# Optimization experiments

Measured on AMD Instinct MI355X. Metric: run time of the kernel, lower is better.

The kernel has to match this reference:

```python
import jax, jax.numpy as jnp
import numpy as np

B, S, E, H, L, F, V = 8, 1024, 768, 12, 6, 3072, 32000
HD = E // H  # head_dim = 64
EPS = 1e-5


def _pos_encoding(max_len, dim):
    pos = np.arange(max_len, dtype=np.float32)[:, None]
    div = np.exp(np.arange(0, dim, 2, dtype=np.float32) * (-np.log(10000.0) / dim))
    pe = np.zeros((max_len, dim), dtype=np.float32)
    pe[:, 0::2] = np.sin(pos * div)
    pe[:, 1::2] = np.cos(pos * div)
    return jnp.asarray(pe)


def setup_inputs() -> dict:
    key = jax.random.key(0)
    ks = jax.random.split(key, 16)
    sd = 0.02
    inp = {}
    inp['input_ids'] = jax.random.randint(ks[0], (B, S), 0, V)
    inp['attention_mask'] = jnp.ones((B, S), dtype=jnp.int32)
    inp['emb'] = jax.random.normal(ks[1], (V, E), jnp.float32) * sd
    inp['pe'] = _pos_encoding(S, E)
    inp['Wq'] = jax.random.normal(ks[2], (L, E, E), jnp.float32) * sd
    inp['bq'] = jnp.zeros((L, E), jnp.float32)
    inp['Wk'] = jax.random.normal(ks[3], (L, E, E), jnp.float32) * sd
    inp['bk'] = jnp.zeros((L, E), jnp.float32)
    inp['Wv'] = jax.random.normal(ks[4], (L, E, E), jnp.float32) * sd
    inp['bv'] = jnp.zeros((L, E), jnp.float32)
    inp['Wo'] = jax.random.normal(ks[5], (L, E, E), jnp.float32) * sd
    inp['bo'] = jnp.zeros((L, E), jnp.float32)
    inp['ln1_g'] = jnp.ones((L, E), jnp.float32)
    inp['ln1_b'] = jnp.zeros((L, E), jnp.float32)
    inp['W1'] = jax.random.normal(ks[6], (L, E, F), jnp.float32) * sd
    inp['b1'] = jnp.zeros((L, F), jnp.float32)
    inp['W2'] = jax.random.normal(ks[7], (L, F, E), jnp.float32) * sd
    inp['b2'] = jnp.zeros((L, E), jnp.float32)
    inp['ln2_g'] = jnp.ones((L, E), jnp.float32)
    inp['ln2_b'] = jnp.zeros((L, E), jnp.float32)
    inp['Wc'] = jax.random.normal(ks[8], (E, 2), jnp.float32) * sd
    inp['bc'] = jnp.zeros((2,), jnp.float32)
    return inp


def _layernorm(x, g, b):
    mu = jnp.mean(x, axis=-1, keepdims=True)
    var = jnp.mean(jnp.square(x - mu), axis=-1, keepdims=True)
    return (x - mu) * jax.lax.rsqrt(var + EPS) * g + b


def reference(input_ids, attention_mask, emb, pe, Wq, bq, Wk, bk, Wv, bv, Wo, bo,
              ln1_g, ln1_b, W1, b1, W2, b2, ln2_g, ln2_b, Wc, bc):
    x = emb[input_ids] + pe[None, :S, :]           # [B,S,E] (dropout = eval identity)
    mask = attention_mask[:, None, None, :]        # [B,1,1,S]
    scale = jnp.sqrt(jnp.float32(HD))

    def block(x, p):
        wq, bq_, wk, bk_, wv, bv_, wo, bo_, g1, be1, w1, b1_, w2, b2_, g2, be2 = p
        q = (x @ wq + bq_).reshape(B, S, H, HD).transpose(0, 2, 1, 3)  # [B,H,S,D]
        k = (x @ wk + bk_).reshape(B, S, H, HD).transpose(0, 2, 1, 3)
        v = (x @ wv + bv_).reshape(B, S, H, HD).transpose(0, 2, 1, 3)
        scores = jnp.einsum('bhsd,bhtd->bhst', q, k) / scale          # [B,H,S,S]
        scores = jnp.where(mask == 0, -jnp.inf, scores)
        attn = jax.nn.softmax(scores, axis=-1)
        o = jnp.einsum('bhst,bhtd->bhsd', attn, v)
        o = o.transpose(0, 2, 1, 3).reshape(B, S, E) @ wo + bo_
        x = _layernorm(x + o, g1, be1)
        ffn = jax.nn.relu(x @ w1 + b1_) @ w2 + b2_
        x = _layernorm(x + ffn, g2, be2)
        return x, None

    params = (Wq, bq, Wk, bk, Wv, bv, Wo, bo, ln1_g, ln1_b, W1, b1, W2, b2, ln2_g, ln2_b)
    x, _ = jax.lax.scan(block, x, params)
    pooled = jnp.mean(x, axis=1)                   # [B,E]
    return pooled @ Wc + bc                        # [B,2]
```

## Files before the change

### kernel.cpp

```cpp
#include <hip/hip_runtime.h>

typedef __bf16 bf16x8 __attribute__((ext_vector_type(8)));
typedef float  f32x4  __attribute__((ext_vector_type(4)));

constexpr int Bb = 8, Ss = 1024, Ee = 768, Hh = 12, Ll = 6, Ff = 3072;
constexpr int TOK  = Bb * Ss;
constexpr int NQKV = 3 * Ee;

static __device__ __forceinline__ f32x4 mfma16(bf16x8 a, bf16x8 b, f32x4 c) {
  return __builtin_amdgcn_mfma_f32_16x16x32_bf16(a, b, c, 0, 0, 0);
}

static __device__ __forceinline__ void async16(const void* g, void* l) {
  __builtin_amdgcn_global_load_lds(
      (const __attribute__((address_space(1))) unsigned int*)g,
      (__attribute__((address_space(3))) unsigned int*)l, 16, 0, 0);
}

static __device__ __forceinline__ bf16x8 ds_read128(const __bf16* p) {
  bf16x8 r;
  unsigned a = (unsigned)(size_t)p;
  asm volatile("ds_read_b128 %0, %1" : "=v"(r) : "v"(a));
  return r;
}

static __device__ __forceinline__ float fexp2(float x) {
  float r; asm("v_exp_f32 %0, %1" : "=v"(r) : "v"(x)); return r;
}

__global__ __launch_bounds__(256) void embed_kernel(
    const int* __restrict__ ids, const float* __restrict__ emb,
    const float* __restrict__ pe, float* __restrict__ x, __bf16* __restrict__ xb)
{
  int tok = blockIdx.x;
  int s   = tok & (Ss - 1);
  int id  = ids[tok];
  const float* er = emb + (size_t)id * Ee;
  const float* pr = pe  + (size_t)s  * Ee;
  size_t base = (size_t)tok * Ee;
#pragma unroll
  for (int i = 0; i < 3; i++) {
    int e = threadIdx.x + i * 256;
    float v = er[e] + pr[e];
    x[base + e]  = v;
    xb[base + e] = (__bf16)v;
  }
}

__global__ __launch_bounds__(256) void transpose_w_kernel(
    const float* __restrict__ src, __bf16* __restrict__ dst,
    int K, int N, size_t sls, size_t dls)
{
  __shared__ float t[32][33];
  src += (size_t)blockIdx.z * sls;
  dst += (size_t)blockIdx.z * dls;
  int n0 = blockIdx.x * 32, k0 = blockIdx.y * 32;
  int c = threadIdx.x & 31, r0 = threadIdx.x >> 5;
#pragma unroll
  for (int rr = 0; rr < 32; rr += 8)
    t[r0 + rr][c] = src[(size_t)(k0 + r0 + rr) * N + n0 + c];
  __syncthreads();
#pragma unroll
  for (int rr = 0; rr < 32; rr += 8)
    dst[(size_t)(n0 + r0 + rr) * K + k0 + c] = (__bf16)t[c][r0 + rr];
}

template<bool OUT_BF16, bool RELU>
__global__ __launch_bounds__(256, 3) void gemm_kernel(
    const __bf16* __restrict__ A, const __bf16* __restrict__ Bt,
    const float* __restrict__ bias0, const float* __restrict__ bias1,
    const float* __restrict__ bias2, int bseg,
    float* __restrict__ Cf, __bf16* __restrict__ Cb, int M, int N, int K)
{
  __shared__ __align__(16) __bf16 lA[3][64 * 64];
  __shared__ __align__(16) __bf16 lB[3][64 * 64];
  const int tid  = threadIdx.x;
  const int wave = tid >> 6, lane = tid & 63;
  const int quad = lane >> 4, c16 = lane & 15;
  const int wm = wave >> 1, wn = wave & 1;

  const int bid = blockIdx.x;
  const int xcd = bid & 7;
  const int lb  = bid >> 3;
  const int mb  = xcd * 8 + (lb & 7);
  const int nb  = lb >> 3;
  const size_t m0 = (size_t)mb * 128, n0 = (size_t)nb * 128;

  f32x4 acc[4][4] = {};

  const int s0l = tid >> 3;
  const int s0c = tid & 7;
  const int l0  = s0c ^ (s0l & 7);
  const int tr0 = (s0l << 1) | (l0 >> 2);
  const int gc0 = (l0 & 3) * 8;
  const int s1l = (tid + 256) >> 3;
  const int l1  = s0c ^ (s1l & 7);
  const int tr1 = (s1l << 1) | (l1 >> 2);
  const int gc1 = (l1 & 3) * 8;

  const __bf16* Ag0 = A  + (m0 + tr0) * K + gc0;
  const __bf16* Ag1 = A  + (m0 + tr1) * K + gc1;
  const __bf16* Bg0 = Bt + (n0 + tr0) * K + gc0;
  const __bf16* Bg1 = Bt + (n0 + tr1) * K + gc1;
  const int d0 = tid * 8;

  const int nk = K >> 5;

  auto stage = [&](int t, int slot) {
    const int kof = t << 5;
    async16(Ag0 + kof, &lA[slot][d0]);
    async16(Ag1 + kof, &lA[slot][d0 + 2048]);
    async16(Bg0 + kof, &lB[slot][d0]);
    async16(Bg1 + kof, &lB[slot][d0 + 2048]);
  };

  int aoff[4], boff[4];
#pragma unroll
  for (int f = 0; f < 4; f++) {
    int ra = wm * 64 + f * 16 + c16;
    int ja = ra >> 1;
    aoff[f] = ja * 64 + (((((ra & 1) << 2) | quad)) ^ (ja & 7)) * 8;
    int rb = wn * 64 + f * 16 + c16;
    int jb = rb >> 1;
    boff[f] = jb * 64 + (((((rb & 1) << 2) | quad)) ^ (jb & 7)) * 8;
  }

  stage(0, 0);
  stage(1, 1);
  asm volatile("s_waitcnt vmcnt(4)" ::: "memory");
  __builtin_amdgcn_s_barrier();
  __builtin_amdgcn_sched_barrier(0);

  int slot = 0;
  for (int t = 0; t < nk; ++t) {
    if (t + 2 < nk) {
      int ns = slot + 2; if (ns >= 3) ns -= 3;
      stage(t + 2, ns);
    }
    const __bf16* la = &lA[slot][0];
    const __bf16* lb = &lB[slot][0];
    bf16x8 af[4], bfr[4];
#pragma unroll
    for (int f = 0; f < 4; f++) af[f]  = ds_read128(la + aoff[f]);
#pragma unroll
    for (int f = 0; f < 4; f++) bfr[f] = ds_read128(lb + boff[f]);
    asm volatile("s_waitcnt lgkmcnt(0)" ::: "memory");
    __builtin_amdgcn_sched_barrier(0);
    __builtin_amdgcn_s_setprio(1);
#pragma unroll
    for (int mi = 0; mi < 4; mi++)
#pragma unroll
      for (int ni = 0; ni < 4; ni++)
        acc[mi][ni] = mfma16(af[mi], bfr[ni], acc[mi][ni]);
    __builtin_amdgcn_s_setprio(0);
    __builtin_amdgcn_sched_barrier(0);
    if (t + 2 < nk) asm volatile("s_waitcnt vmcnt(4)" ::: "memory");
    else            asm volatile("s_waitcnt vmcnt(0)" ::: "memory");
    __builtin_amdgcn_s_barrier();
    __builtin_amdgcn_sched_barrier(0);
    slot = (slot + 1 == 3) ? 0 : slot + 1;
  }

#pragma unroll
  for (int ni = 0; ni < 4; ni++) {
    int col = (int)n0 + wn * 64 + ni * 16 + c16;
    const float* bp = bias0;
    int cc = col;
    if (cc >= bseg) { bp = bias1; cc -= bseg; }
    if (cc >= bseg) { bp = bias2; cc -= bseg; }
    float bv = bp[cc];
#pragma unroll
    for (int mi = 0; mi < 4; mi++) {
#pragma unroll
      for (int rr = 0; rr < 4; rr++) {
        size_t row = m0 + wm * 64 + mi * 16 + quad * 4 + rr;
        float v = acc[mi][ni][rr] + bv;
        if (RELU) v = fmaxf(v, 0.f);
        if (OUT_BF16) Cb[row * N + col] = (__bf16)v;
        else          Cf[row * N + col] = v;
      }
    }
  }
}

__global__ __launch_bounds__(256, 4) void gemm64_kernel(
    const __bf16* __restrict__ A, const __bf16* __restrict__ Bt,
    const float* __restrict__ bias0,
    float* __restrict__ Cf, int N, int K)
{
  __shared__ __align__(16) __bf16 lA[3][32 * 64];
  __shared__ __align__(16) __bf16 lB[3][64 * 64];
  const int tid  = threadIdx.x;
  const int lane = tid & 63, wn = tid >> 6;
  const int quad = lane >> 4, c16 = lane & 15;

  const int bid = blockIdx.x;
  const int xcd = bid & 7;
  const int lb  = bid >> 3;
  const int mb  = xcd * 16 + (lb & 15);
  const int nb  = lb >> 4;
  const size_t m0 = (size_t)mb * 64, n0 = (size_t)nb * 128;

  f32x4 acc[4][2] = {};

  const int alr = tid >> 3, asc = tid & 7;
  const int al  = asc ^ (alr & 7);
  const int atr = (alr << 1) | (al >> 2);
  const int agc = (al & 3) * 8;
  const __bf16* Ag = A + (m0 + atr) * (size_t)K + agc;
  const int s0l = tid >> 3;
  const int s0c = tid & 7;
  const int l0  = s0c ^ (s0l & 7);
  const int tr0 = (s0l << 1) | (l0 >> 2);
  const int gc0 = (l0 & 3) * 8;
  const int s1l = (tid + 256) >> 3;
  const int l1  = s0c ^ (s1l & 7);
  const int tr1 = (s1l << 1) | (l1 >> 2);
  const int gc1 = (l1 & 3) * 8;
  const __bf16* Bg0 = Bt + (n0 + tr0) * (size_t)K + gc0;
  const __bf16* Bg1 = Bt + (n0 + tr1) * (size_t)K + gc1;
  const int d0 = tid * 8;

  const int nk = K >> 5;

  auto stage = [&](int t, int slot) {
    const int kof = t << 5;
    async16(Ag  + kof, &lA[slot][d0]);
    async16(Bg0 + kof, &lB[slot][d0]);
    async16(Bg1 + kof, &lB[slot][d0 + 2048]);
  };

  int aoff[4], boff[2];
#pragma unroll
  for (int f = 0; f < 4; f++) {
    int ra = f * 16 + c16;
    int ja = ra >> 1;
    aoff[f] = ja * 64 + ((((ra & 1) << 2) | quad) ^ (ja & 7)) * 8;
  }
#pragma unroll
  for (int f = 0; f < 2; f++) {
    int rb = wn * 32 + f * 16 + c16;
    int jb = rb >> 1;
    boff[f] = jb * 64 + ((((rb & 1) << 2) | quad) ^ (jb & 7)) * 8;
  }

  stage(0, 0);
  stage(1, 1);
  asm volatile("s_waitcnt vmcnt(3)" ::: "memory");
  __builtin_amdgcn_s_barrier();
  __builtin_amdgcn_sched_barrier(0);

  int slot = 0;
  for (int t = 0; t < nk; ++t) {
    if (t + 2 < nk) {
      int ns = slot + 2; if (ns >= 3) ns -= 3;
      stage(t + 2, ns);
    }
    const __bf16* la = &lA[slot][0];
    const __bf16* lb = &lB[slot][0];
    bf16x8 af[4], bfr[2];
#pragma unroll
    for (int f = 0; f < 4; f++) af[f]  = ds_read128(la + aoff[f]);
#pragma unroll
    for (int f = 0; f < 2; f++) bfr[f] = ds_read128(lb + boff[f]);
    asm volatile("s_waitcnt lgkmcnt(0)" ::: "memory");
    __builtin_amdgcn_sched_barrier(0);
    __builtin_amdgcn_s_setprio(1);
#pragma unroll
    for (int mi = 0; mi < 4; mi++)
#pragma unroll
      for (int ni = 0; ni < 2; ni++)
        acc[mi][ni] = mfma16(af[mi], bfr[ni], acc[mi][ni]);
    __builtin_amdgcn_s_setprio(0);
    __builtin_amdgcn_sched_barrier(0);
    if (t + 2 < nk) asm volatile("s_waitcnt vmcnt(3)" ::: "memory");
    else            asm volatile("s_waitcnt vmcnt(0)" ::: "memory");
    __builtin_amdgcn_s_barrier();
    __builtin_amdgcn_sched_barrier(0);
    slot = (slot + 1 == 3) ? 0 : slot + 1;
  }

#pragma unroll
  for (int ni = 0; ni < 2; ni++) {
    int col = (int)n0 + wn * 32 + ni * 16 + c16;
    float bv = bias0[col];
#pragma unroll
    for (int mi = 0; mi < 4; mi++) {
#pragma unroll
      for (int rr = 0; rr < 4; rr++) {
        size_t row = m0 + mi * 16 + quad * 4 + rr;
        Cf[row * N + col] = acc[mi][ni][rr] + bv;
      }
    }
  }
}

__global__ __launch_bounds__(256) void vtrans_kernel(
    const __bf16* __restrict__ qkv, __bf16* __restrict__ vt)
{
  int tid  = blockIdx.x * 256 + threadIdx.x;
  int d    = tid & 63;
  int rest = tid >> 6;
  int sc   = rest & 127;
  int bh   = rest >> 7;
  int b = bh / Hh, h = bh % Hh;
  const __bf16* src = qkv + (size_t)(b * Ss + sc * 8) * NQKV + 2 * Ee + h * 64 + d;
  bf16x8 v;
#pragma unroll
  for (int i = 0; i < 8; i++) v[i] = src[(size_t)i * NQKV];
  *(bf16x8*)(vt + ((size_t)bh * 64 + d) * Ss + sc * 8) = v;
}

__global__ __launch_bounds__(512, 6) void attn_kernel(
    const __bf16* __restrict__ qkv, const __bf16* __restrict__ vt,
    const int* __restrict__ amask, __bf16* __restrict__ out)
{
  __shared__ __align__(16) __bf16 kbuf[2][64 * 64];
  __shared__ __align__(16) __bf16 vbuf[2][64 * 64];
  __shared__ __align__(16) __bf16 plds[8][16 * 68];
  const int idx = blockIdx.x;
  const int bh = idx % 96, qi = idx / 96;
  const int b = bh / Hh, h = bh % Hh;
  const int lane = threadIdx.x & 63, wave = threadIdx.x >> 6;
  const int quad = lane >> 4, c16 = lane & 15;
  const int q0 = qi * 128 + wave * 16;

  const __bf16* qbase = qkv + (size_t)(b * Ss + q0 + c16) * NQKV + h * 64 + quad * 8;
  bf16x8 qf0 = *(const bf16x8*)(qbase);
  bf16x8 qf1 = *(const bf16x8*)(qbase + 32);

  const int srow = threadIdx.x >> 3;
  const int scol = ((threadIdx.x & 7) ^ (srow & 7)) * 8;
  const __bf16* kg = qkv + (size_t)(b * Ss + srow) * NQKV + Ee + h * 64 + scol;
  const __bf16* vg = vt + ((size_t)bh * 64 + srow) * Ss + scol;

  const int sa8 = c16 & 7;
  const int rc0 = (quad ^ sa8) * 8;
  const int rc1 = ((quad + 4) ^ sa8) * 8;

  f32x4 o[4] = {};
  float lrow[4] = {0.f, 0.f, 0.f, 0.f};
  const int* mp = amask + b * Ss;
  __bf16* pw = &plds[wave][0];
  const float CE = 0.18033688f;

  async16(kg, &kbuf[0][(size_t)threadIdx.x * 8]);
  async16(vg, &vbuf[0][(size_t)threadIdx.x * 8]);

  for (int t = 0; t < 16; t++) {
    const int tb = t * 64;
    __syncthreads();
    if (t < 15) {
      const int nb = (t + 1) & 1, ntb = tb + 64;
      async16(kg + (size_t)ntb * NQKV, &kbuf[nb][(size_t)threadIdx.x * 8]);
      async16(vg + ntb,                &vbuf[nb][(size_t)threadIdx.x * 8]);
    }
    const __bf16* kb = &kbuf[t & 1][0];
    const __bf16* vb = &vbuf[t & 1][0];

    float mk2[4];
#pragma unroll
    for (int n = 0; n < 4; n++) mk2[n] = mp[tb + n * 16 + c16] ? 0.f : -1e30f;
    bf16x8 kf[8], vf[8];
#pragma unroll
    for (int n = 0; n < 4; n++) {
      kf[2*n]   = *(const bf16x8*)(kb + (n * 16 + c16) * 64 + rc0);
      kf[2*n+1] = *(const bf16x8*)(kb + (n * 16 + c16) * 64 + rc1);
    }
#pragma unroll
    for (int n = 0; n < 4; n++) {
      vf[2*n]   = *(const bf16x8*)(vb + (n * 16 + c16) * 64 + rc0);
      vf[2*n+1] = *(const bf16x8*)(vb + (n * 16 + c16) * 64 + rc1);
    }

    f32x4 s[4];
#pragma unroll
    for (int n = 0; n < 4; n++) {
      f32x4 z = {};
      z = mfma16(qf0, kf[2*n], z);
      s[n] = mfma16(qf1, kf[2*n+1], z);
    }

#pragma unroll
    for (int rr = 0; rr < 4; rr++) {
      float p0 = fexp2(fmaf(s[0][rr], CE, mk2[0]));
      float p1 = fexp2(fmaf(s[1][rr], CE, mk2[1]));
      float p2 = fexp2(fmaf(s[2][rr], CE, mk2[2]));
      float p3 = fexp2(fmaf(s[3][rr], CE, mk2[3]));
      lrow[rr] += (p0 + p1) + (p2 + p3);
      int prow = (quad * 4 + rr) * 68;
      pw[prow + 0  + c16] = (__bf16)p0;
      pw[prow + 16 + c16] = (__bf16)p1;
      pw[prow + 32 + c16] = (__bf16)p2;
      pw[prow + 48 + c16] = (__bf16)p3;
    }

    bf16x8 pf0 = *(const bf16x8*)(pw + c16 * 68 + quad * 8);
    bf16x8 pf1 = *(const bf16x8*)(pw + c16 * 68 + 32 + quad * 8);
#pragma unroll
    for (int ni = 0; ni < 4; ni++) {
      o[ni] = mfma16(pf0, vf[2*ni],   o[ni]);
      o[ni] = mfma16(pf1, vf[2*ni+1], o[ni]);
    }
  }

#pragma unroll
  for (int rr = 0; rr < 4; rr++) {
    float sr = lrow[rr];
    sr += __shfl_xor(sr, 1);
    sr += __shfl_xor(sr, 2);
    sr += __shfl_xor(sr, 4);
    sr += __shfl_xor(sr, 8);
    float inv = 1.f / sr;
    size_t row = (size_t)(b * Ss + q0 + quad * 4 + rr) * Ee + h * 64;
    out[row + 0  + c16] = (__bf16)(o[0][rr] * inv);
    out[row + 16 + c16] = (__bf16)(o[1][rr] * inv);
    out[row + 32 + c16] = (__bf16)(o[2][rr] * inv);
    out[row + 48 + c16] = (__bf16)(o[3][rr] * inv);
  }
}

__global__ __launch_bounds__(256) void add_ln_kernel(
    const float* __restrict__ xin, const float* __restrict__ tmp,
    const float* __restrict__ g, const float* __restrict__ beta,
    float* __restrict__ xout, __bf16* __restrict__ xbout)
{
  __shared__ float red[8];
  size_t base = (size_t)blockIdx.x * Ee;
  float hv[3], s = 0.f, sq = 0.f;
#pragma unroll
  for (int i = 0; i < 3; i++) {
    int e = threadIdx.x + i * 256;
    hv[i] = xin[base + e] + tmp[base + e];
    s += hv[i]; sq += hv[i] * hv[i];
  }
#pragma unroll
  for (int m = 1; m < 64; m <<= 1) { s += __shfl_xor(s, m); sq += __shfl_xor(sq, m); }
  int wave = threadIdx.x >> 6;
  if ((threadIdx.x & 63) == 0) { red[wave] = s; red[4 + wave] = sq; }
  __syncthreads();
  s  = red[0] + red[1] + red[2] + red[3];
  sq = red[4] + red[5] + red[6] + red[7];
  float mean = s * (1.f / Ee);
  float var  = sq * (1.f / Ee) - mean * mean;
  float rstd = rsqrtf(var + 1e-5f);
#pragma unroll
  for (int i = 0; i < 3; i++) {
    int e = threadIdx.x + i * 256;
    float v = (hv[i] - mean) * rstd * g[e] + beta[e];
    xout[base + e]  = v;
    xbout[base + e] = (__bf16)v;
  }
}

__global__ __launch_bounds__(256) void pool1_kernel(
    const float* __restrict__ x, float* __restrict__ partial)
{
  int b = blockIdx.x, chunk = blockIdx.y;
  float acc[3] = {0.f, 0.f, 0.f};
  for (int s = chunk * 64; s < chunk * 64 + 64; s++) {
#pragma unroll
    for (int i = 0; i < 3; i++) {
      int e = threadIdx.x + i * 256;
      acc[i] += x[((size_t)b * Ss + s) * Ee + e];
    }
  }
#pragma unroll
  for (int i = 0; i < 3; i++) {
    int e = threadIdx.x + i * 256;
    partial[((size_t)b * 16 + chunk) * Ee + e] = acc[i];
  }
}

__global__ __launch_bounds__(256) void pool2_kernel(
    const float* __restrict__ partial, const float* __restrict__ Wc,
    const float* __restrict__ bc, float* __restrict__ out)
{
  __shared__ float red[8];
  int b = blockIdx.x;
  float p0 = 0.f, p1 = 0.f;
#pragma unroll
  for (int i = 0; i < 3; i++) {
    int e = threadIdx.x + i * 256;
    float pe_ = 0.f;
#pragma unroll
    for (int c = 0; c < 16; c++) pe_ += partial[((size_t)b * 16 + c) * Ee + e];
    pe_ *= (1.f / Ss);
    p0 += pe_ * Wc[e * 2 + 0];
    p1 += pe_ * Wc[e * 2 + 1];
  }
#pragma unroll
  for (int m = 1; m < 64; m <<= 1) { p0 += __shfl_xor(p0, m); p1 += __shfl_xor(p1, m); }
  int wave = threadIdx.x >> 6;
  if ((threadIdx.x & 63) == 0) { red[wave] = p0; red[4 + wave] = p1; }
  __syncthreads();
  if (threadIdx.x == 0) {
    out[b * 2 + 0] = red[0] + red[1] + red[2] + red[3] + bc[0];
    out[b * 2 + 1] = red[4] + red[5] + red[6] + red[7] + bc[1];
  }
}

extern "C" void kernel_launch(void* const* d_in, const int* in_sizes, int n_in,
                              void* d_out, int out_size, void* d_ws, size_t ws_size,
                              hipStream_t stream) {
  const int*   ids   = (const int*)  d_in[0];
  const int*   amask = (const int*)  d_in[1];
  const float* emb   = (const float*)d_in[2];
  const float* pe    = (const float*)d_in[3];
  const float* Wq    = (const float*)d_in[4];
  const float* bq    = (const float*)d_in[5];
  const float* Wk    = (const float*)d_in[6];
  const float* bk    = (const float*)d_in[7];
  const float* Wv    = (const float*)d_in[8];
  const float* bv    = (const float*)d_in[9];
  const float* Wo    = (const float*)d_in[10];
  const float* bo    = (const float*)d_in[11];
  const float* ln1g  = (const float*)d_in[12];
  const float* ln1b  = (const float*)d_in[13];
  const float* W1    = (const float*)d_in[14];
  const float* b1    = (const float*)d_in[15];
  const float* W2    = (const float*)d_in[16];
  const float* b2    = (const float*)d_in[17];
  const float* ln2g  = (const float*)d_in[18];
  const float* ln2b  = (const float*)d_in[19];
  const float* Wc    = (const float*)d_in[20];
  const float* bc    = (const float*)d_in[21];
  float* outp = (float*)d_out;

  char* p = (char*)d_ws;
  auto alloc = [&](size_t bytes) { char* r = p; p += (bytes + 255) & ~(size_t)255; return r; };
  float*  x     = (float*) alloc((size_t)TOK * Ee * 4);
  __bf16* xb    = (__bf16*)alloc((size_t)TOK * Ee * 2);
  float*  tmp   = (float*) alloc((size_t)TOK * Ee * 4);
  __bf16* attn  = (__bf16*)alloc((size_t)TOK * Ee * 2);
  char*   r1    = alloc((size_t)TOK * Ff * 2);
  __bf16* qkv   = (__bf16*)r1;
  __bf16* vt    = (__bf16*)(r1 + (size_t)TOK * NQKV * 2);
  __bf16* h1    = (__bf16*)r1;
  __bf16* wqkvt = (__bf16*)alloc((size_t)Ll * NQKV * Ee * 2);
  __bf16* wot   = (__bf16*)alloc((size_t)Ll * Ee * Ee * 2);
  __bf16* w1t   = (__bf16*)alloc((size_t)Ll * Ff * Ee * 2);
  __bf16* w2t   = (__bf16*)alloc((size_t)Ll * Ee * Ff * 2);
  float*  part  = (float*) alloc((size_t)Bb * 16 * Ee * 4);

  embed_kernel<<<TOK, 256, 0, stream>>>(ids, emb, pe, x, xb);

  transpose_w_kernel<<<dim3(Ee/32, Ee/32, Ll), 256, 0, stream>>>(
      Wq, wqkvt,                         Ee, Ee, (size_t)Ee*Ee, (size_t)NQKV*Ee);
  transpose_w_kernel<<<dim3(Ee/32, Ee/32, Ll), 256, 0, stream>>>(
      Wk, wqkvt + (size_t)Ee*Ee,         Ee, Ee, (size_t)Ee*Ee, (size_t)NQKV*Ee);
  transpose_w_kernel<<<dim3(Ee/32, Ee/32, Ll), 256, 0, stream>>>(
      Wv, wqkvt + (size_t)2*Ee*Ee,       Ee, Ee, (size_t)Ee*Ee, (size_t)NQKV*Ee);
  transpose_w_kernel<<<dim3(Ee/32, Ee/32, Ll), 256, 0, stream>>>(
      Wo, wot,                           Ee, Ee, (size_t)Ee*Ee, (size_t)Ee*Ee);
  transpose_w_kernel<<<dim3(Ff/32, Ee/32, Ll), 256, 0, stream>>>(
      W1, w1t,                           Ee, Ff, (size_t)Ee*Ff, (size_t)Ff*Ee);
  transpose_w_kernel<<<dim3(Ee/32, Ff/32, Ll), 256, 0, stream>>>(
      W2, w2t,                           Ff, Ee, (size_t)Ff*Ee, (size_t)Ee*Ff);

  for (int l = 0; l < Ll; l++) {
    gemm_kernel<true, false><<<64 * (NQKV/128), 256, 0, stream>>>(
        xb, wqkvt + (size_t)l*NQKV*Ee,
        bq + l*Ee, bk + l*Ee, bv + l*Ee, Ee,
        nullptr, qkv, TOK, NQKV, Ee);
    vtrans_kernel<<<3072, 256, 0, stream>>>(qkv, vt);
    attn_kernel<<<768, 512, 0, stream>>>(qkv, vt, amask, attn);
    gemm64_kernel<<<768, 256, 0, stream>>>(
        attn, wot + (size_t)l*Ee*Ee, bo + l*Ee, tmp, Ee, Ee);
    add_ln_kernel<<<TOK, 256, 0, stream>>>(x, tmp, ln1g + l*Ee, ln1b + l*Ee, x, xb);
    gemm_kernel<true, true><<<64 * (Ff/128), 256, 0, stream>>>(
        xb, w1t + (size_t)l*Ff*Ee,
        b1 + l*Ff, b1 + l*Ff, b1 + l*Ff, Ff,
        nullptr, h1, TOK, Ff, Ee);
    gemm64_kernel<<<768, 256, 0, stream>>>(
        h1, w2t + (size_t)l*Ee*Ff, b2 + l*Ee, tmp, Ee, Ff);
    add_ln_kernel<<<TOK, 256, 0, stream>>>(x, tmp, ln2g + l*Ee, ln2b + l*Ee, x, xb);
  }

  pool1_kernel<<<dim3(Bb, 16), 256, 0, stream>>>(x, part);
  pool2_kernel<<<Bb, 256, 0, stream>>>(part, Wc, bc, outp);
}
```

Before: 1.989 ms.

## Replace 64x128 4-wave N=768 GEMM with 128x128 8-wave tile kernel

```diff
diff --git a/kernel.cpp b/kernel.cpp
--- a/kernel.cpp
+++ b/kernel.cpp
@@ -183,70 +183,60 @@
   }
 }
 
-__global__ __launch_bounds__(256, 4) void gemm64_kernel(
+__global__ __launch_bounds__(512, 6) void gemm8w_kernel(
     const __bf16* __restrict__ A, const __bf16* __restrict__ Bt,
     const float* __restrict__ bias0,
     float* __restrict__ Cf, int N, int K)
 {
-  __shared__ __align__(16) __bf16 lA[3][32 * 64];
+  __shared__ __align__(16) __bf16 lA[3][64 * 64];
   __shared__ __align__(16) __bf16 lB[3][64 * 64];
   const int tid  = threadIdx.x;
-  const int lane = tid & 63, wn = tid >> 6;
+  const int wave = tid >> 6, lane = tid & 63;
   const int quad = lane >> 4, c16 = lane & 15;
+  const int wm = wave >> 1, wn = wave & 1;
 
   const int bid = blockIdx.x;
   const int xcd = bid & 7;
   const int lb  = bid >> 3;
-  const int mb  = xcd * 16 + (lb & 15);
-  const int nb  = lb >> 4;
-  const size_t m0 = (size_t)mb * 64, n0 = (size_t)nb * 128;
-
-  f32x4 acc[4][2] = {};
-
-  const int alr = tid >> 3, asc = tid & 7;
-  const int al  = asc ^ (alr & 7);
-  const int atr = (alr << 1) | (al >> 2);
-  const int agc = (al & 3) * 8;
-  const __bf16* Ag = A + (m0 + atr) * (size_t)K + agc;
-  const int s0l = tid >> 3;
-  const int s0c = tid & 7;
-  const int l0  = s0c ^ (s0l & 7);
-  const int tr0 = (s0l << 1) | (l0 >> 2);
-  const int gc0 = (l0 & 3) * 8;
-  const int s1l = (tid + 256) >> 3;
-  const int l1  = s0c ^ (s1l & 7);
-  const int tr1 = (s1l << 1) | (l1 >> 2);
-  const int gc1 = (l1 & 3) * 8;
-  const __bf16* Bg0 = Bt + (n0 + tr0) * (size_t)K + gc0;
-  const __bf16* Bg1 = Bt + (n0 + tr1) * (size_t)K + gc1;
+  const int mb  = xcd * 8 + (lb & 7);
+  const int nb  = lb >> 3;
+  const size_t m0 = (size_t)mb * 128, n0 = (size_t)nb * 128;
+
+  f32x4 acc[2][4] = {};
+
+  const int slr = tid >> 3, ssc = tid & 7;
+  const int sl  = ssc ^ (slr & 7);
+  const int str = (slr << 1) | (sl >> 2);
+  const int sgc = (sl & 3) * 8;
+  const __bf16* Ag = A  + (m0 + str) * (size_t)K + sgc;
+  const __bf16* Bg = Bt + (n0 + str) * (size_t)K + sgc;
   const int d0 = tid * 8;
 
   const int nk = K >> 5;
 
   auto stage = [&](int t, int slot) {
     const int kof = t << 5;
-    async16(Ag  + kof, &lA[slot][d0]);
-    async16(Bg0 + kof, &lB[slot][d0]);
-    async16(Bg1 + kof, &lB[slot][d0 + 2048]);
+    async16(Ag + kof, &lA[slot][d0]);
+    async16(Bg + kof, &lB[slot][d0]);
   };
 
-  int aoff[4], boff[2];
-#pragma unroll
-  for (int f = 0; f < 4; f++) {
-    int ra = f * 16 + c16;
+  int aoff[2], boff[4];
+#pragma unroll
+  for (int f = 0; f < 2; f++) {
+    int ra = wm * 32 + f * 16 + c16;
     int ja = ra >> 1;
     aoff[f] = ja * 64 + ((((ra & 1) << 2) | quad) ^ (ja & 7)) * 8;
   }
 #pragma unroll
-  for (int f = 0; f < 2; f++) {
-    int rb = wn * 32 + f * 16 + c16;
+  for (int f = 0; f < 4; f++) {
+    int rb = wn * 64 + f * 16 + c16;
     int jb = rb >> 1;
     boff[f] = jb * 64 + ((((rb & 1) << 2) | quad) ^ (jb & 7)) * 8;
   }
 
   stage(0, 0);
   stage(1, 1);
-  asm volatile("s_waitcnt vmcnt(3)" ::: "memory");
+  asm volatile("s_waitcnt vmcnt(2)" ::: "memory");
   __builtin_amdgcn_s_barrier();
   __builtin_amdgcn_sched_barrier(0);
 
@@ -258,22 +248,22 @@
     }
     const __bf16* la = &lA[slot][0];
     const __bf16* lb = &lB[slot][0];
-    bf16x8 af[4], bfr[2];
-#pragma unroll
-    for (int f = 0; f < 4; f++) af[f]  = ds_read128(la + aoff[f]);
-#pragma unroll
-    for (int f = 0; f < 2; f++) bfr[f] = ds_read128(lb + boff[f]);
+    bf16x8 af[2], bfr[4];
+#pragma unroll
+    for (int f = 0; f < 2; f++) af[f]  = ds_read128(la + aoff[f]);
+#pragma unroll
+    for (int f = 0; f < 4; f++) bfr[f] = ds_read128(lb + boff[f]);
     asm volatile("s_waitcnt lgkmcnt(0)" ::: "memory");
     __builtin_amdgcn_sched_barrier(0);
     __builtin_amdgcn_s_setprio(1);
 #pragma unroll
-    for (int mi = 0; mi < 4; mi++)
-#pragma unroll
-      for (int ni = 0; ni < 2; ni++)
+    for (int mi = 0; mi < 2; mi++)
+#pragma unroll
+      for (int ni = 0; ni < 4; ni++)
         acc[mi][ni] = mfma16(af[mi], bfr[ni], acc[mi][ni]);
     __builtin_amdgcn_s_setprio(0);
     __builtin_amdgcn_sched_barrier(0);
-    if (t + 2 < nk) asm volatile("s_waitcnt vmcnt(3)" ::: "memory");
+    if (t + 2 < nk) asm volatile("s_waitcnt vmcnt(2)" ::: "memory");
     else            asm volatile("s_waitcnt vmcnt(0)" ::: "memory");
     __builtin_amdgcn_s_barrier();
     __builtin_amdgcn_sched_barrier(0);
@@ -281,14 +271,14 @@
   }
 
 #pragma unroll
-  for (int ni = 0; ni < 2; ni++) {
-    int col = (int)n0 + wn * 32 + ni * 16 + c16;
+  for (int ni = 0; ni < 4; ni++) {
+    int col = (int)n0 + wn * 64 + ni * 16 + c16;
     float bv = bias0[col];
 #pragma unroll
-    for (int mi = 0; mi < 4; mi++) {
+    for (int mi = 0; mi < 2; mi++) {
 #pragma unroll
       for (int rr = 0; rr < 4; rr++) {
-        size_t row = m0 + mi * 16 + quad * 4 + rr;
+        size_t row = m0 + wm * 32 + mi * 16 + quad * 4 + rr;
         Cf[row * N + col] = acc[mi][ni][rr] + bv;
       }
     }
@@ -565,14 +555,14 @@
         nullptr, qkv, TOK, NQKV, Ee);
     vtrans_kernel<<<3072, 256, 0, stream>>>(qkv, vt);
     attn_kernel<<<768, 512, 0, stream>>>(qkv, vt, amask, attn);
-    gemm64_kernel<<<768, 256, 0, stream>>>(
+    gemm8w_kernel<<<64 * (Ee/128), 512, 0, stream>>>(
         attn, wot + (size_t)l*Ee*Ee, bo + l*Ee, tmp, Ee, Ee);
     add_ln_kernel<<<TOK, 256, 0, stream>>>(x, tmp, ln1g + l*Ee, ln1b + l*Ee, x, xb);
     gemm_kernel<true, true><<<64 * (Ff/128), 256, 0, stream>>>(
         xb, w1t + (size_t)l*Ff*Ee,
         b1 + l*Ff, b1 + l*Ff, b1 + l*Ff, Ff,
         nullptr, h1, TOK, Ff, Ee);
-    gemm64_kernel<<<768, 256, 0, stream>>>(
+    gemm8w_kernel<<<64 * (Ee/128), 512, 0, stream>>>(
         h1, w2t + (size_t)l*Ee*Ff, b2 + l*Ee, tmp, Ee, Ff);
     add_ln_kernel<<<TOK, 256, 0, stream>>>(x, tmp, ln2g + l*Ee, ln2b + l*Ee, x, xb);
   }
```

Result: faster. 1.899 ms (-4.5%).
